# Optimization experiments

Measured on AMD Instinct MI355X. Metric: run time of the kernel, lower is better.

## Reference

```python
import jax, jax.numpy as jnp
import numpy as np

B, P, D = 8, 1024, 1024
H, N = 16, 64  # num_heads, head_dim


def setup_inputs() -> dict:
    key = jax.random.key(0)
    k1, k2, k3 = jax.random.split(key, 3)
    inputs = jax.random.normal(k1, (B, P, D), dtype=jnp.float32)
    # Keras 'random_normal' initializer: stddev 0.05
    w_qkv = jax.random.normal(k2, (H, 3, D, N), dtype=jnp.float32) * 0.05
    w_o = jax.random.normal(k3, (N * H, D), dtype=jnp.float32) * 0.05
    return {"inputs": inputs, "w_qkv": w_qkv, "w_o": w_o}


def reference(inputs, w_qkv, w_o):
    # Per-head QKV projection: [b,p,d] x [h,3,d,n] -> [b,h,3,p,n]
    proj = jnp.einsum('bpv,havn->bhapn', inputs, w_qkv)
    q = proj[:, :, 0]  # [b,h,p,n]
    k = proj[:, :, 1]
    v = proj[:, :, 2]
    head_dim = q.shape[-1]
    scale = 1.0 / jnp.sqrt(jnp.asarray(head_dim, dtype=jnp.float32))
    scores = jnp.einsum('bhqn,bhkn->bhqk', q, k) * scale  # [b,h,p,p]
    attn = jax.nn.softmax(scores, axis=-1)
    out = jnp.einsum('bhqk,bhkn->bhqn', attn, v)  # [b,h,p,n]
    # concat heads along feature dim: [b,p,h*n]
    b, h, p, n = out.shape
    concat = out.transpose(0, 2, 1, 3).reshape(b, p, h * n)
    return jnp.einsum('bpi,ij->bpj', concat, w_o)  # [b,p,d_model]
```

## Files before the change

### kernel.cpp

```cpp
#include <hip/hip_runtime.h>
#include <stdint.h>

typedef _Float16 f16;
typedef __attribute__((ext_vector_type(2))) _Float16 f16x2;
typedef __attribute__((ext_vector_type(4))) _Float16 f16x4;
typedef __attribute__((ext_vector_type(8))) _Float16 f16x8;
typedef __attribute__((ext_vector_type(2))) __fp16 h16x2;
typedef __attribute__((ext_vector_type(4))) float f32x4;
typedef __attribute__((ext_vector_type(4))) uint32_t u32x4;

__device__ __forceinline__ void gload_lds16(const void* g, void* l) {
  __builtin_amdgcn_global_load_lds(
      (__attribute__((address_space(1))) void*)const_cast<void*>(g),
      (__attribute__((address_space(3))) void*)l, 16, 0, 0);
}


__global__ void convert_x(const float* __restrict__ in, f16* __restrict__ out) {
  int i = blockIdx.x * 256 + threadIdx.x;
  float4 v = ((const float4*)in)[i];
  f16x4 hv;
  hv[0] = (f16)v.x; hv[1] = (f16)v.y; hv[2] = (f16)v.z; hv[3] = (f16)v.w;
  ((f16x4*)out)[i] = hv;
}

__global__ void transpose_wqkv(const float* __restrict__ in, f16* __restrict__ out) {
  __shared__ float tile[64][65];
  int s = blockIdx.x >> 4;
  int vt = blockIdx.x & 15;
  int hh = s / 3, a = s - hh * 3;
  int tx = threadIdx.x & 63, ty = threadIdx.x >> 6;
#pragma unroll
  for (int i = 0; i < 16; i++) {
    int r = i * 4 + ty;
    tile[r][tx] = in[((size_t)(s * 1024 + vt * 64 + r)) * 64 + tx];
  }
  __syncthreads();
#pragma unroll
  for (int i = 0; i < 16; i++) {
    int n = i * 4 + ty;
    out[((size_t)(a * 1024 + hh * 64 + n)) * 1024 + vt * 64 + tx] = (f16)tile[tx][n];
  }
}

__global__ void transpose_wo(const float* __restrict__ in, f16* __restrict__ out) {
  __shared__ float tile[64][65];
  int rt = blockIdx.x >> 4, ct = blockIdx.x & 15;
  int tx = threadIdx.x & 63, ty = threadIdx.x >> 6;
#pragma unroll
  for (int i = 0; i < 16; i++) {
    int r = i * 4 + ty;
    tile[r][tx] = in[((size_t)(rt * 64 + r)) * 1024 + ct * 64 + tx];
  }
  __syncthreads();
#pragma unroll
  for (int i = 0; i < 16; i++) {
    int j = i * 4 + ty;
    out[((size_t)(ct * 64 + j)) * 1024 + rt * 64 + tx] = (f16)tile[tx][j];
  }
}

template <int OUTMODE>
__global__ __launch_bounds__(256, 2) void gemm_kernel(
    const f16* __restrict__ A, const f16* __restrict__ BT, void* __restrict__ out,
    void* __restrict__ out2, int M, int N, int K) {
  __shared__ __align__(16) f16 As[128][64];
  __shared__ __align__(16) f16 Bs[128][64];
  const int t = threadIdx.x;
  const int lane = t & 63, wave = t >> 6;
  const int lr = lane & 15, lg = lane >> 4;
  const int wm = wave >> 1, wn = wave & 1;
  const int nTN = N >> 7;
  const int bm = blockIdx.x / nTN, bn = blockIdx.x % nTN;
  const f16* Ab = A + (size_t)bm * 128 * K;
  const f16* Bb = BT + (size_t)bn * 128 * K;

  const f32x4 zero4 = {0.f, 0.f, 0.f, 0.f};
  f32x4 acc[4][4];
#pragma unroll
  for (int m = 0; m < 4; m++)
#pragma unroll
    for (int n = 0; n < 4; n++) acc[m][n] = zero4;

  for (int k0 = 0; k0 < K; k0 += 64) {
    __syncthreads();
#pragma unroll
    for (int i = 0; i < 4; i++) {
      int q = wave * 4 + i;
      int u = q * 64 + lane;
      int r = u >> 3, j = u & 7;
      gload_lds16(Ab + (size_t)r * K + k0 + ((j ^ (r & 7)) << 3),
                  (char*)&As[0][0] + q * 1024);
      gload_lds16(Bb + (size_t)r * K + k0 + ((j ^ (r & 7)) << 3),
                  (char*)&Bs[0][0] + q * 1024);
    }
    __syncthreads();
#pragma unroll
    for (int half = 0; half < 2; half++) {
      f16x8 af[4], bf[4];
#pragma unroll
      for (int m = 0; m < 4; m++) {
        int r = wm * 64 + m * 16 + lr;
        af[m] = *(const f16x8*)&As[r][((half * 4 + lg) ^ (r & 7)) << 3];
      }
#pragma unroll
      for (int n = 0; n < 4; n++) {
        int r = wn * 64 + n * 16 + lr;
        bf[n] = *(const f16x8*)&Bs[r][((half * 4 + lg) ^ (r & 7)) << 3];
      }
#pragma unroll
      for (int m = 0; m < 4; m++)
#pragma unroll
        for (int n = 0; n < 4; n++)
          acc[m][n] = __builtin_amdgcn_mfma_f32_16x16x32_f16(af[m], bf[n], acc[m][n], 0, 0, 0);
    }
  }

  const int r0 = bm * 128 + wm * 64;
  const int c0 = bn * 128 + wn * 64;
  if (OUTMODE == 2 && bn >= 16) {
    f16* VT = (f16*)out2;
    const int bb = bm >> 3;
#pragma unroll
    for (int m = 0; m < 4; m++) {
      int pl = (r0 + m * 16 + lg * 4) & 1023;
      int pl2 = (pl & 992) | ((pl & 12) << 1) | ((pl & 16) >> 2);
#pragma unroll
      for (int n = 0; n < 4; n++) {
        int vcol = c0 - 2048 + n * 16 + lr;
        f16x4 pv;
#pragma unroll
        for (int i = 0; i < 4; i++) pv[i] = (f16)acc[m][n][i];
        *(f16x4*)&VT[((size_t)(bb * 16 + (vcol >> 6)) * 64 + (vcol & 63)) * 1024 + pl2] = pv;
      }
    }
  } else {
#pragma unroll
    for (int m = 0; m < 4; m++)
#pragma unroll
      for (int n = 0; n < 4; n++)
#pragma unroll
        for (int i = 0; i < 4; i++) {
          int gr = r0 + m * 16 + lg * 4 + i;
          int gc = c0 + n * 16 + lr;
          if (OUTMODE == 1)
            ((float*)out)[(size_t)gr * N + gc] = acc[m][n][i];
          else
            ((f16*)out)[(size_t)gr * N + gc] = (f16)acc[m][n][i];
        }
  }
}

__global__ __launch_bounds__(256, 4) void attn_kernel(
    const f16* __restrict__ QKV, const f16* __restrict__ VT, f16* __restrict__ C) {
  __shared__ __align__(16) f16 smem[16384];

  const int t = threadIdx.x, lane = t & 63, wave = t >> 6;
  const int lr = lane & 15, lg = lane >> 4;
  const int pt = blockIdx.x, bh = blockIdx.y;
  const int b = bh >> 4, h = bh & 15;
  const int p0 = pt * 128;

  const f16* Qg = QKV + ((size_t)(b * 1024 + p0)) * 3072 + h * 64;
  const f16* Kg = QKV + ((size_t)(b * 1024)) * 3072 + 1024 + h * 64;
  const f16* Vg = VT + (size_t)bh * 64 * 1024;

#pragma unroll
  for (int i = 0; i < 4; i++) {
    int q = wave * 4 + i;
    int u = q * 64 + lane;
    int r = u >> 3, j = u & 7;
    gload_lds16(Qg + (size_t)r * 3072 + ((j ^ (r & 7)) << 3), (char*)smem + q * 1024);
  }
  __syncthreads();

  const f16 qscale = (f16)0.180336878f;
  f16x8 qa[2][2];
#pragma unroll
  for (int m = 0; m < 2; m++)
#pragma unroll
    for (int hh = 0; hh < 2; hh++) {
      int r = wave * 32 + m * 16 + lr;
      f16x8 v = *(const f16x8*)&smem[(size_t)r * 64 + (((hh * 4 + lg) ^ (lr & 7)) << 3)];
#pragma unroll
      for (int e = 0; e < 8; e++) v[e] *= qscale;
      qa[m][hh] = v;
    }
  __syncthreads();

  auto STAGE = [&](int kc, int cur) {
#pragma unroll
    for (int i = 0; i < 2; i++) {
      int q = wave * 2 + i;
      int u = q * 64 + lane;
      int r = u >> 3, j = u & 7;
      gload_lds16(Kg + (size_t)(kc * 64 + r) * 3072 + ((j ^ (r & 7)) << 3),
                  (char*)smem + cur * 16384 + q * 1024);
      gload_lds16(Vg + (size_t)r * 1024 + kc * 64 + ((j ^ (r & 7)) << 3),
                  (char*)smem + cur * 16384 + 8192 + q * 1024);
    }
  };

  STAGE(0, 0);
  STAGE(1, 1);
  __syncthreads();

  const f32x4 zero4 = {0.f, 0.f, 0.f, 0.f};
  f32x4 o[2][4], o_l[2];
#pragma unroll
  for (int m = 0; m < 2; m++) {
    o_l[m] = zero4;
#pragma unroll
    for (int n = 0; n < 4; n++) o[m][n] = zero4;
  }
  float mrun[2] = {0.f, 0.f};
  const f16x8 ones8 = {(f16)1.f, (f16)1.f, (f16)1.f, (f16)1.f,
                       (f16)1.f, (f16)1.f, (f16)1.f, (f16)1.f};

#pragma unroll 1
  for (int kc = 0; kc < 16; kc++) {
    const int cur = kc & 1;
    const int kB = cur * 8192;
    const char* vB = (const char*)smem + cur * 16384 + 8192;

    f32x4 s[2][4];
#pragma unroll
    for (int m = 0; m < 2; m++) {
      f32x4 init = {-mrun[m], -mrun[m], -mrun[m], -mrun[m]};
#pragma unroll
      for (int kb = 0; kb < 4; kb++) s[m][kb] = init;
    }
    __builtin_amdgcn_s_setprio(1);
#pragma unroll
    for (int kb = 0; kb < 4; kb++) {
      int r = kb * 16 + lr;
      f16x8 kf0 = *(const f16x8*)&smem[kB + (size_t)r * 64 + ((lg ^ (lr & 7)) << 3)];
      f16x8 kf1 = *(const f16x8*)&smem[kB + (size_t)r * 64 + (((4 + lg) ^ (lr & 7)) << 3)];
#pragma unroll
      for (int m = 0; m < 2; m++) {
        s[m][kb] = __builtin_amdgcn_mfma_f32_16x16x32_f16(kf0, qa[m][0], s[m][kb], 0, 0, 0);
        s[m][kb] = __builtin_amdgcn_mfma_f32_16x16x32_f16(kf1, qa[m][1], s[m][kb], 0, 0, 0);
      }
    }
    __builtin_amdgcn_s_setprio(0);

    f16x8 pa8[2][2];
#pragma unroll
    for (int m = 0; m < 2; m++) {
      float mx = fmaxf(fmaxf(fmaxf(s[m][0][0], s[m][0][1]), fmaxf(s[m][0][2], s[m][0][3])),
                       fmaxf(fmaxf(s[m][1][0], s[m][1][1]), fmaxf(s[m][1][2], s[m][1][3])));
      mx = fmaxf(mx, fmaxf(fmaxf(fmaxf(s[m][2][0], s[m][2][1]), fmaxf(s[m][2][2], s[m][2][3])),
                           fmaxf(fmaxf(s[m][3][0], s[m][3][1]), fmaxf(s[m][3][2], s[m][3][3]))));
      mx = fmaxf(mx, __shfl_xor(mx, 16));
      mx = fmaxf(mx, __shfl_xor(mx, 32));
      if (__any(mx > 4.328085f)) {
        float delta = fmaxf(mx, 0.f);
        mrun[m] += delta;
        float alpha = exp2f(-delta);
#pragma unroll
        for (int kb = 0; kb < 4; kb++)
#pragma unroll
          for (int i = 0; i < 4; i++) s[m][kb][i] -= delta;
#pragma unroll
        for (int i = 0; i < 4; i++) {
          float ai = __shfl(alpha, (lane & 48) | (lg * 4 + i));
          o_l[m][i] *= ai;
#pragma unroll
          for (int n = 0; n < 4; n++) o[m][n][i] *= ai;
        }
      }
#pragma unroll
      for (int j = 0; j < 2; j++) {
        uint32_t w0, w1, w2, w3;
        w0 = __builtin_bit_cast(uint32_t, __builtin_amdgcn_cvt_pkrtz(exp2f(s[m][2 * j][0]), exp2f(s[m][2 * j][1])));
        w1 = __builtin_bit_cast(uint32_t, __builtin_amdgcn_cvt_pkrtz(exp2f(s[m][2 * j][2]), exp2f(s[m][2 * j][3])));
        w2 = __builtin_bit_cast(uint32_t, __builtin_amdgcn_cvt_pkrtz(exp2f(s[m][2 * j + 1][0]), exp2f(s[m][2 * j + 1][1])));
        w3 = __builtin_bit_cast(uint32_t, __builtin_amdgcn_cvt_pkrtz(exp2f(s[m][2 * j + 1][2]), exp2f(s[m][2 * j + 1][3])));
        u32x4 ww = {w0, w1, w2, w3};
        pa8[m][j] = __builtin_bit_cast(f16x8, ww);
      }
    }

    __builtin_amdgcn_s_setprio(1);
#pragma unroll
    for (int j = 0; j < 2; j++) {
      o_l[0] = __builtin_amdgcn_mfma_f32_16x16x32_f16(pa8[0][j], ones8, o_l[0], 0, 0, 0);
      o_l[1] = __builtin_amdgcn_mfma_f32_16x16x32_f16(pa8[1][j], ones8, o_l[1], 0, 0, 0);
#pragma unroll
      for (int n = 0; n < 4; n++) {
        int rv = n * 16 + lr;
        f16x8 vb = *(const f16x8*)(vB + (size_t)rv * 128 + (((4 * j + lg) ^ (lr & 7)) << 4));
        o[0][n] = __builtin_amdgcn_mfma_f32_16x16x32_f16(pa8[0][j], vb, o[0][n], 0, 0, 0);
        o[1][n] = __builtin_amdgcn_mfma_f32_16x16x32_f16(pa8[1][j], vb, o[1][n], 0, 0, 0);
      }
    }
    __builtin_amdgcn_s_setprio(0);

    __syncthreads();
    if (kc + 2 < 16) STAGE(kc + 2, cur);
  }

#pragma unroll
  for (int m = 0; m < 2; m++)
#pragma unroll
    for (int i = 0; i < 4; i++) {
      float li = 1.f / o_l[m][i];
      int prow = p0 + wave * 32 + m * 16 + lg * 4 + i;
#pragma unroll
      for (int n = 0; n < 4; n++) {
        int col = h * 64 + n * 16 + lr;
        C[((size_t)(b * 1024 + prow)) * 1024 + col] = (f16)(o[m][n][i] * li);
      }
    }
}

extern "C" void kernel_launch(void* const* d_in, const int* in_sizes, int n_in,
                              void* d_out, int out_size, void* d_ws, size_t ws_size,
                              hipStream_t stream) {
  const float* X = (const float*)d_in[0];
  const float* Wqkv = (const float*)d_in[1];
  const float* Wo = (const float*)d_in[2];
  float* Y = (float*)d_out;

  f16* ws = (f16*)d_ws;
  f16* X16 = ws;
  f16* WqkvT = ws + 8388608;
  f16* WoT = ws + 11534336;
  f16* QKV = ws + 12582912;
  f16* VT = (f16*)d_out;

  convert_x<<<8192, 256, 0, stream>>>(X, X16);
  transpose_wqkv<<<768, 256, 0, stream>>>(Wqkv, WqkvT);
  transpose_wo<<<256, 256, 0, stream>>>(Wo, WoT);
  gemm_kernel<2><<<64 * 24, 256, 0, stream>>>(X16, WqkvT, QKV, VT, 8192, 3072, 1024);
  attn_kernel<<<dim3(8, 128), 256, 0, stream>>>(QKV, VT, X16 );
  gemm_kernel<1><<<64 * 8, 256, 0, stream>>>(X16 , WoT, Y, nullptr, 8192, 1024, 1024);
}
```

Baseline: 173.3 us.

## Fuse fp32-to-fp16 input conversion into the QKV GEMM A-tile load

Removes the separate convert_x kernel. The QKV GEMM now reads fp32 X directly into registers, converts it with packed RTZ conversion, and writes swizzled fp16 into LDS. The next tile's A load is issued early, overlapping it with the MFMA loop. This drops a full read and write pass over the 32MB input, but the GEMM now re-reads fp32 A once per N-tile (24 times), which costs more bandwidth, and it adds register pressure. Also raises launch_bounds occupancy to 4 and adds s_setprio around the MFMA blocks.

```diff
diff --git a/kernel.cpp b/kernel.cpp
--- a/kernel.cpp
+++ b/kernel.cpp
@@ -2,10 +2,8 @@
 #include <stdint.h>
 
 typedef _Float16 f16;
-typedef __attribute__((ext_vector_type(2))) _Float16 f16x2;
 typedef __attribute__((ext_vector_type(4))) _Float16 f16x4;
 typedef __attribute__((ext_vector_type(8))) _Float16 f16x8;
-typedef __attribute__((ext_vector_type(2))) __fp16 h16x2;
 typedef __attribute__((ext_vector_type(4))) float f32x4;
 typedef __attribute__((ext_vector_type(4))) uint32_t u32x4;
 
@@ -15,14 +13,6 @@
       (__attribute__((address_space(3))) void*)l, 16, 0, 0);
 }
 
-
-__global__ void convert_x(const float* __restrict__ in, f16* __restrict__ out) {
-  int i = blockIdx.x * 256 + threadIdx.x;
-  float4 v = ((const float4*)in)[i];
-  f16x4 hv;
-  hv[0] = (f16)v.x; hv[1] = (f16)v.y; hv[2] = (f16)v.z; hv[3] = (f16)v.w;
-  ((f16x4*)out)[i] = hv;
-}
 
 __global__ void transpose_wqkv(const float* __restrict__ in, f16* __restrict__ out) {
   __shared__ float tile[64][65];
@@ -60,9 +50,9 @@
   }
 }
 
-template <int OUTMODE>
-__global__ __launch_bounds__(256, 2) void gemm_kernel(
-    const f16* __restrict__ A, const f16* __restrict__ BT, void* __restrict__ out,
+template <int OUTMODE, int AF32>
+__global__ __launch_bounds__(256, 4) void gemm_kernel(
+    const void* __restrict__ Ap, const f16* __restrict__ BT, void* __restrict__ out,
     void* __restrict__ out2, int M, int N, int K) {
   __shared__ __align__(16) f16 As[128][64];
   __shared__ __align__(16) f16 Bs[128][64];
@@ -72,7 +62,8 @@
   const int wm = wave >> 1, wn = wave & 1;
   const int nTN = N >> 7;
   const int bm = blockIdx.x / nTN, bn = blockIdx.x % nTN;
-  const f16* Ab = A + (size_t)bm * 128 * K;
+  const f16* Ab16 = (const f16*)Ap + (size_t)bm * 128 * K;
+  const float* Abf = (const float*)Ap + (size_t)bm * 128 * K;
   const f16* Bb = BT + (size_t)bn * 128 * K;
 
   const f32x4 zero4 = {0.f, 0.f, 0.f, 0.f};
@@ -82,19 +73,50 @@
 #pragma unroll
     for (int n = 0; n < 4; n++) acc[m][n] = zero4;
 
+  float4 aR[8];
+  auto LOADA = [&](int k0) {
+#pragma unroll
+    for (int i = 0; i < 8; i++) {
+      int u = i * 256 + t;
+      int r = u >> 4, c = u & 15;
+      aR[i] = *(const float4*)(Abf + (size_t)r * K + k0 + c * 4);
+    }
+  };
+  if (AF32) LOADA(0);
+
   for (int k0 = 0; k0 < K; k0 += 64) {
     __syncthreads();
+    if (AF32) {
+#pragma unroll
+      for (int i = 0; i < 8; i++) {
+        int u = i * 256 + t;
+        int r = u >> 4, c = u & 15;
+        int j = c >> 1, half = c & 1;
+        uint32_t lo = __builtin_bit_cast(uint32_t, __builtin_amdgcn_cvt_pkrtz(aR[i].x, aR[i].y));
+        uint32_t hi = __builtin_bit_cast(uint32_t, __builtin_amdgcn_cvt_pkrtz(aR[i].z, aR[i].w));
+        uint2 w = {lo, hi};
+        *(uint2*)((char*)&As[0][0] + r * 128 + ((j ^ (r & 7)) << 4) + half * 8) = w;
+      }
+    } else {
+#pragma unroll
+      for (int i = 0; i < 4; i++) {
+        int q = wave * 4 + i;
+        int u = q * 64 + lane;
+        int r = u >> 3, j = u & 7;
+        gload_lds16(Ab16 + (size_t)r * K + k0 + ((j ^ (r & 7)) << 3),
+                    (char*)&As[0][0] + q * 1024);
+      }
+    }
 #pragma unroll
     for (int i = 0; i < 4; i++) {
       int q = wave * 4 + i;
       int u = q * 64 + lane;
       int r = u >> 3, j = u & 7;
-      gload_lds16(Ab + (size_t)r * K + k0 + ((j ^ (r & 7)) << 3),
-                  (char*)&As[0][0] + q * 1024);
       gload_lds16(Bb + (size_t)r * K + k0 + ((j ^ (r & 7)) << 3),
                   (char*)&Bs[0][0] + q * 1024);
     }
     __syncthreads();
+    if (AF32 && k0 + 64 < K) LOADA(k0 + 64);
 #pragma unroll
     for (int half = 0; half < 2; half++) {
       f16x8 af[4], bf[4];
@@ -108,11 +130,13 @@
         int r = wn * 64 + n * 16 + lr;
         bf[n] = *(const f16x8*)&Bs[r][((half * 4 + lg) ^ (r & 7)) << 3];
       }
+      __builtin_amdgcn_s_setprio(1);
 #pragma unroll
       for (int m = 0; m < 4; m++)
 #pragma unroll
         for (int n = 0; n < 4; n++)
           acc[m][n] = __builtin_amdgcn_mfma_f32_16x16x32_f16(af[m], bf[n], acc[m][n], 0, 0, 0);
+      __builtin_amdgcn_s_setprio(0);
     }
   }
 
@@ -323,16 +347,15 @@
   float* Y = (float*)d_out;
 
   f16* ws = (f16*)d_ws;
-  f16* X16 = ws;
+  f16* C16 = ws;
   f16* WqkvT = ws + 8388608;
   f16* WoT = ws + 11534336;
   f16* QKV = ws + 12582912;
   f16* VT = (f16*)d_out;
 
-  convert_x<<<8192, 256, 0, stream>>>(X, X16);
   transpose_wqkv<<<768, 256, 0, stream>>>(Wqkv, WqkvT);
   transpose_wo<<<256, 256, 0, stream>>>(Wo, WoT);
-  gemm_kernel<2><<<64 * 24, 256, 0, stream>>>(X16, WqkvT, QKV, VT, 8192, 3072, 1024);
-  attn_kernel<<<dim3(8, 128), 256, 0, stream>>>(QKV, VT, X16 );
-  gemm_kernel<1><<<64 * 8, 256, 0, stream>>>(X16 , WoT, Y, nullptr, 8192, 1024, 1024);
-}
+  gemm_kernel<2, 1><<<64 * 24, 256, 0, stream>>>(X, WqkvT, QKV, VT, 8192, 3072, 1024);
+  attn_kernel<<<dim3(8, 128), 256, 0, stream>>>(QKV, VT, C16);
+  gemm_kernel<1, 0><<<64 * 8, 256, 0, stream>>>(C16, WoT, Y, nullptr, 8192, 1024, 1024);
+}
```

New measurement: 420.6 us. +142.8%, slower.
